# Kernel optimization log

Hardware: AMD Instinct MI355X
Metric: run time of the kernel (lower is better)

## Reference

```python
import jax, jax.numpy as jnp
import numpy as np

B, T, C, H, E, K = 4, 2048, 1024, 2048, 8, 2


def setup_inputs() -> dict:
    key = jax.random.key(0)
    ks = jax.random.split(key, 9)
    s = lambda k, shape, fan: jax.random.normal(k, shape, jnp.float32) / np.sqrt(fan)
    return {
        "x": jax.random.normal(ks[0], (B, T, C), jnp.float32),
        "gate_w": s(ks[1], (C, E), C),            # router gate (no bias)
        "sg_w": s(ks[2], (C, H), C),              # shared expert: gate proj
        "su_w": s(ks[3], (C, H), C),              # shared expert: up proj
        "sd_w": s(ks[4], (H, C), H),              # shared expert: down proj
        "eg_w": s(ks[5], (E, C, H), C),           # routed experts: gate proj
        "eu_w": s(ks[6], (E, C, H), C),           # routed experts: up proj
        "ed_w": s(ks[7], (E, H, C), H),           # routed experts: down proj
    }


def _swiglu(x, wg, wu, wd):
    # x: (B,T,C) -> (B,T,C)
    return jnp.einsum("bth,hc->btc", jax.nn.silu(jnp.einsum("btc,ch->bth", x, wg)) * jnp.einsum("btc,ch->bth", x, wu), wd)


def reference(x, gate_w, sg_w, su_w, sd_w, eg_w, eu_w, ed_w):
    # Router: top-k over expert logits, softmax over selected logits
    logits = jnp.einsum("btc,ce->bte", x, gate_w)            # (B,T,E)
    topk_logits, topk_idx = jax.lax.top_k(logits, K)         # (B,T,K)
    weights = jax.nn.softmax(topk_logits, axis=-1)           # (B,T,K)
    # Dense per-expert combine weight: w_e[b,t,e] = sum_k weights*(idx==e)
    onehot = jax.nn.one_hot(topk_idx, E, dtype=x.dtype)      # (B,T,K,E)
    dense_w = jnp.einsum("btk,btke->bte", weights, onehot)   # (B,T,E)

    shared_out = _swiglu(x, sg_w, su_w, sd_w)

    # Scan over experts (small fixed E), accumulating weighted expert outputs.
    dense_w_e = jnp.moveaxis(dense_w, -1, 0)                 # (E,B,T)

    def step(acc, params):
        wg, wu, wd, w = params
        return acc + w[..., None] * _swiglu(x, wg, wu, wd), None

    expert_out, _ = jax.lax.scan(step, jnp.zeros_like(x), (eg_w, eu_w, ed_w, dense_w_e))
    return shared_out + expert_out, logits
```

## Files before the change

kernel.cpp:

```cpp
#include <hip/hip_runtime.h>
#include <cstdint>
#include <cstddef>

#define NTOK 8192
#define CDIM 1024
#define HDIM 2048
#define NEXP 8
#define NSEG 9
#define MAXTILES 104

typedef __bf16 bf16;
typedef unsigned short u16;
typedef __attribute__((ext_vector_type(8))) __bf16 bf16x8;
typedef __attribute__((ext_vector_type(4))) float f32x4;

__device__ __forceinline__ u16 f2bf(float f) {
  union { u16 u; __bf16 b; } cv;
  cv.b = (__bf16)f;
  return cv.u;
}

__device__ __forceinline__ void gload_lds16(const bf16* g, bf16* l) {
  __builtin_amdgcn_global_load_lds(
      (const __attribute__((address_space(1))) unsigned int*)g,
      (__attribute__((address_space(3))) unsigned int*)l, 16, 0, 0);
}

__global__ __launch_bounds__(64) void init_kernel(int* __restrict__ counts,
                                                  int* __restrict__ fill) {
  if (threadIdx.x < NEXP) {
    counts[threadIdx.x] = 0;
    fill[threadIdx.x] = 0;
  }
}

__global__ __launch_bounds__(256) void cast_x_kernel(
    const float* __restrict__ src, bf16* __restrict__ dst) {
  size_t i = ((size_t)blockIdx.x * 256 + threadIdx.x) * 8;
  float4 a = *(const float4*)(src + i);
  float4 b = *(const float4*)(src + i + 4);
  bf16x8 p;
  p[0] = (bf16)a.x; p[1] = (bf16)a.y; p[2] = (bf16)a.z; p[3] = (bf16)a.w;
  p[4] = (bf16)b.x; p[5] = (bf16)b.y; p[6] = (bf16)b.z; p[7] = (bf16)b.w;
  *(bf16x8*)(dst + i) = p;
}

__global__ __launch_bounds__(256) void router2_kernel(
    const float* __restrict__ x, const float* __restrict__ gw,
    float* __restrict__ logits_out, int* __restrict__ tk_e,
    float* __restrict__ tk_w, int* __restrict__ counts) {
  int wv = threadIdx.x >> 6, l = threadIdx.x & 63;
  int t = blockIdx.x * 4 + wv;
  const float* xr = x + (size_t)t * CDIM;
  float acc[NEXP];
#pragma unroll
  for (int e = 0; e < NEXP; ++e) acc[e] = 0.f;
  for (int c = l; c < CDIM; c += 64) {
    float xv = xr[c];
    const float* g = gw + (size_t)c * NEXP;
    float4 g0 = *(const float4*)(g);
    float4 g1 = *(const float4*)(g + 4);
    acc[0] += xv * g0.x; acc[1] += xv * g0.y; acc[2] += xv * g0.z; acc[3] += xv * g0.w;
    acc[4] += xv * g1.x; acc[5] += xv * g1.y; acc[6] += xv * g1.z; acc[7] += xv * g1.w;
  }
#pragma unroll
  for (int off = 32; off > 0; off >>= 1) {
#pragma unroll
    for (int e = 0; e < NEXP; ++e) acc[e] += __shfl_xor(acc[e], off, 64);
  }
  int e0 = 0; float l0 = acc[0];
#pragma unroll
  for (int e = 1; e < NEXP; ++e) { if (acc[e] > l0) { l0 = acc[e]; e0 = e; } }
  int e1 = -1; float l1 = -3.4e38f;
#pragma unroll
  for (int e = 0; e < NEXP; ++e) { if (e != e0 && acc[e] > l1) { l1 = acc[e]; e1 = e; } }
  float ex = expf(l1 - l0);
  float w0 = 1.f / (1.f + ex), w1 = ex / (1.f + ex);
  if (l < NEXP) logits_out[(size_t)t * NEXP + l] = acc[l];
  if (l == 0) {
    tk_e[2 * t] = e0; tk_e[2 * t + 1] = e1;
    tk_w[2 * t] = w0; tk_w[2 * t + 1] = w1;
    atomicAdd(&counts[e0], 1);
    atomicAdd(&counts[e1], 1);
  }
}

__global__ __launch_bounds__(256) void offsets_kernel(
    const int* __restrict__ counts, int* __restrict__ offs_g,
    int* __restrict__ tile_seg, int* __restrict__ list_tok) {
  __shared__ int off[NSEG], pad[NSEG], cnt[NSEG], ntot;
  int tid = threadIdx.x;
  if (tid == 0) {
    int tot = 0;
    for (int e = 0; e < NSEG; ++e) {
      int c = (e < NEXP) ? counts[e] : NTOK;
      cnt[e] = c; off[e] = tot;
      int p = (c + 255) & ~255;
      pad[e] = p; tot += p;
    }
    ntot = tot;
  }
  __syncthreads();
  if (tid < NSEG) offs_g[tid] = off[tid];
  for (int gt = tid; gt < MAXTILES; gt += 256) {
    int row = gt * 256, seg = -1;
    if (row < ntot) {
      for (int e = 0; e < NSEG; ++e)
        if (row >= off[e] && row < off[e] + pad[e]) { seg = e; break; }
    }
    tile_seg[gt] = seg;
  }
  for (int e = 0; e < NSEG; ++e)
    for (int i = off[e] + cnt[e] + tid; i < off[e] + pad[e]; i += 256)
      list_tok[i] = 0;
}

__global__ __launch_bounds__(256) void scatter_kernel(
    const int* __restrict__ tk_e, const int* __restrict__ offs,
    int* __restrict__ fill, int* __restrict__ list_tok,
    int* __restrict__ inv) {
  int t = blockIdx.x * 256 + threadIdx.x;
  int e0 = tk_e[2 * t], e1 = tk_e[2 * t + 1];
  int p0 = atomicAdd(&fill[e0], 1);
  int i0 = offs[e0] + p0;
  list_tok[i0] = t; inv[2 * t] = i0;
  int p1 = atomicAdd(&fill[e1], 1);
  int i1 = offs[e1] + p1;
  list_tok[i1] = t; inv[2 * t + 1] = i1;
  list_tok[offs[NEXP] + t] = t;
}

__device__ __forceinline__ void transpose_body(const float* __restrict__ src,
                                               u16* __restrict__ dst, int R, int C) {
  __shared__ uint32_t t32[64 * 33];
  const int tid = threadIdx.x;
  const int r0 = blockIdx.y * 64, c0 = blockIdx.x * 64;
  const int rp = tid >> 3;
  const int cg = tid & 7;
  const float* s0 = src + (size_t)(r0 + 2 * rp) * C + c0 + 8 * cg;
  const float* s1 = s0 + C;
  float4 a0 = *(const float4*)(s0);
  float4 a1 = *(const float4*)(s0 + 4);
  float4 b0 = *(const float4*)(s1);
  float4 b1 = *(const float4*)(s1 + 4);
  uint32_t p[8];
  p[0] = f2bf(a0.x) | ((uint32_t)f2bf(b0.x) << 16);
  p[1] = f2bf(a0.y) | ((uint32_t)f2bf(b0.y) << 16);
  p[2] = f2bf(a0.z) | ((uint32_t)f2bf(b0.z) << 16);
  p[3] = f2bf(a0.w) | ((uint32_t)f2bf(b0.w) << 16);
  p[4] = f2bf(a1.x) | ((uint32_t)f2bf(b1.x) << 16);
  p[5] = f2bf(a1.y) | ((uint32_t)f2bf(b1.y) << 16);
  p[6] = f2bf(a1.z) | ((uint32_t)f2bf(b1.z) << 16);
  p[7] = f2bf(a1.w) | ((uint32_t)f2bf(b1.w) << 16);
#pragma unroll
  for (int c = 0; c < 8; ++c) t32[(8 * cg + c) * 33 + rp] = p[c];
  __syncthreads();
  const int oc = tid >> 2, og = tid & 3;
  const uint32_t* rb = &t32[oc * 33 + 8 * og];
  union { uint32_t w[8]; uint4 v[2]; } u;
#pragma unroll
  for (int k = 0; k < 8; ++k) u.w[k] = rb[k];
  u16* d = dst + (size_t)(c0 + oc) * R + r0 + 16 * og;
  *(uint4*)d = u.v[0];
  *(uint4*)(d + 8) = u.v[1];
}

__global__ __launch_bounds__(256) void transpose_cast_kernel(
    const float* __restrict__ src, u16* __restrict__ dst, int R, int C) {
  transpose_body(src, dst, R, C);
}

__global__ __launch_bounds__(256) void transpose_gu_kernel(
    const float* __restrict__ sg, const float* __restrict__ su,
    const float* __restrict__ eg, const float* __restrict__ eu,
    u16* __restrict__ wTg, u16* __restrict__ wTu) {
  const size_t slot = (size_t)HDIM * CDIM;
  int z = blockIdx.z;
  const float* src; u16* dst;
  if (z == 0)       { src = sg;                 dst = wTg + 8 * slot; }
  else if (z == 1)  { src = su;                 dst = wTu + 8 * slot; }
  else if (z < 10)  { src = eg + (z - 2) * slot;  dst = wTg + (z - 2) * slot; }
  else              { src = eu + (z - 10) * slot; dst = wTu + (z - 10) * slot; }
  transpose_body(src, dst, CDIM, HDIM);
}

__global__ __launch_bounds__(256) void transpose_d_kernel(
    const float* __restrict__ sd, const float* __restrict__ ed,
    u16* __restrict__ wTd) {
  const size_t slot = (size_t)HDIM * CDIM;
  int z = blockIdx.z;
  const float* src; u16* dst;
  if (z == 0) { src = sd;                 dst = wTd + 8 * slot; }
  else        { src = ed + (z - 1) * slot; dst = wTd + (z - 1) * slot; }
  transpose_body(src, dst, HDIM, CDIM);
}


__global__ __launch_bounds__(512, 2) void gemm_gu4(
    const bf16* __restrict__ xb, const bf16* __restrict__ wTg,
    const bf16* __restrict__ wTu, const int* __restrict__ tile_seg,
    const int* __restrict__ list_tok, bf16* __restrict__ act) {
  __shared__ __align__(16) bf16 sS[2][32768];
  __shared__ int tokLds[256];

  const int nwg = gridDim.x;
  const int bid = blockIdx.x;
  const int wid = (bid & 7) * (nwg >> 3) + (bid >> 3);
  const int tileIdx = wid % MAXTILES;
  const int colIdx = wid / MAXTILES;
  const int seg = tile_seg[tileIdx];
  if (seg < 0) return;

  const int tid = threadIdx.x, l = tid & 63, wv = tid >> 6;
  const int wr = wv >> 2, wn = wv & 3;
  const int n0 = colIdx * 128;
  const size_t rowbase = (size_t)tileIdx * 256;

  if (tid < 256) tokLds[tid] = list_tok[rowbase + tid];
  __syncthreads();

  const int row8 = tid >> 3;
  const int scol = (((tid & 7) ^ (row8 & 7)) << 3);
  const bf16* gA0 = xb + (size_t)tokLds[row8] * CDIM + scol;
  const bf16* gA1 = xb + (size_t)tokLds[128 + row8] * CDIM + scol;
  const bf16* gA2 = xb + (size_t)tokLds[64 + row8] * CDIM + scol;
  const bf16* gA3 = xb + (size_t)tokLds[192 + row8] * CDIM + scol;
  const size_t wslot = (size_t)seg * HDIM * CDIM;
  const bf16* gBg = wTg + wslot + (size_t)(n0 + row8) * CDIM + scol;
  const bf16* gBu = wTu + wslot + (size_t)(n0 + row8) * CDIM + scol;
  const int t8 = tid * 8;

  const int fr = l & 15, kq = l >> 4;
  const int cS0 = ((kq ^ (l & 7)) << 4);
  const int cS1 = (((4 | kq) ^ (l & 7)) << 4);
  const int aBase = (wr * 128 + fr) * 128;
  const int gBase = 32768 + (wn * 32 + fr) * 128;
  const int uBase = 49152 + (wn * 32 + fr) * 128;

  f32x4 accG[2][4][2], accU[2][4][2];
#pragma unroll
  for (int h = 0; h < 2; ++h)
#pragma unroll
    for (int i = 0; i < 4; ++i)
#pragma unroll
      for (int j = 0; j < 2; ++j) {
        accG[h][i][j] = (f32x4){0.f, 0.f, 0.f, 0.f};
        accU[h][i][j] = (f32x4){0.f, 0.f, 0.f, 0.f};
      }

  auto stC0 = [&](int b, int k0) { bf16* d = &sS[b][0];
    gload_lds16(gBg + k0, d + 16384 + t8);
    gload_lds16(gBg + 64 * CDIM + k0, d + 20480 + t8); };
  auto stC1 = [&](int b, int k0) { bf16* d = &sS[b][0];
    gload_lds16(gA0 + k0, d + t8);
    gload_lds16(gA1 + k0, d + 8192 + t8); };
  auto stC2 = [&](int b, int k0) { bf16* d = &sS[b][0];
    gload_lds16(gBu + k0, d + 24576 + t8);
    gload_lds16(gBu + 64 * CDIM + k0, d + 28672 + t8); };
  auto stC3 = [&](int b, int k0) { bf16* d = &sS[b][0];
    gload_lds16(gA2 + k0, d + 4096 + t8);
    gload_lds16(gA3 + k0, d + 12288 + t8); };

  constexpr int NKT = CDIM / 64;
  stC0(0, 0); stC1(0, 0); stC2(0, 0); stC3(0, 0);

  for (int kt = 0; kt < NKT; ++kt) {
    const int b = kt & 1, bn = b ^ 1;
    const int kn = (kt + 1) * 64;
    const bool more = (kt + 1 < NKT);
    const char* pS = (const char*)&sS[b][0];
    bf16x8 af[4][2], bg[2][2], bu[2][2];

    asm volatile("s_waitcnt vmcnt(4)" ::: "memory");
    __builtin_amdgcn_s_barrier();
#pragma unroll
    for (int i = 0; i < 4; ++i) {
      af[i][0] = *(const bf16x8*)(pS + aBase + i * 2048 + cS0);
      af[i][1] = *(const bf16x8*)(pS + aBase + i * 2048 + cS1);
    }
#pragma unroll
    for (int j = 0; j < 2; ++j) {
      bg[j][0] = *(const bf16x8*)(pS + gBase + j * 2048 + cS0);
      bg[j][1] = *(const bf16x8*)(pS + gBase + j * 2048 + cS1);
    }
    if (more) stC0(bn, kn);
    asm volatile("s_waitcnt lgkmcnt(0)" ::: "memory");
    __builtin_amdgcn_sched_barrier(0);
    __builtin_amdgcn_s_setprio(1);
#pragma unroll
    for (int i = 0; i < 4; ++i)
#pragma unroll
      for (int j = 0; j < 2; ++j) {
        accG[0][i][j] = __builtin_amdgcn_mfma_f32_16x16x32_bf16(af[i][0], bg[j][0], accG[0][i][j], 0, 0, 0);
        accG[0][i][j] = __builtin_amdgcn_mfma_f32_16x16x32_bf16(af[i][1], bg[j][1], accG[0][i][j], 0, 0, 0);
      }
    __builtin_amdgcn_s_setprio(0);

    if (more) asm volatile("s_waitcnt vmcnt(4)" ::: "memory");
    else      asm volatile("s_waitcnt vmcnt(2)" ::: "memory");
    __builtin_amdgcn_s_barrier();
#pragma unroll
    for (int j = 0; j < 2; ++j) {
      bu[j][0] = *(const bf16x8*)(pS + uBase + j * 2048 + cS0);
      bu[j][1] = *(const bf16x8*)(pS + uBase + j * 2048 + cS1);
    }
    if (more) stC1(bn, kn);
    asm volatile("s_waitcnt lgkmcnt(0)" ::: "memory");
    __builtin_amdgcn_sched_barrier(0);
    __builtin_amdgcn_s_setprio(1);
#pragma unroll
    for (int i = 0; i < 4; ++i)
#pragma unroll
      for (int j = 0; j < 2; ++j) {
        accU[0][i][j] = __builtin_amdgcn_mfma_f32_16x16x32_bf16(af[i][0], bu[j][0], accU[0][i][j], 0, 0, 0);
        accU[0][i][j] = __builtin_amdgcn_mfma_f32_16x16x32_bf16(af[i][1], bu[j][1], accU[0][i][j], 0, 0, 0);
      }
    __builtin_amdgcn_s_setprio(0);

    if (more) asm volatile("s_waitcnt vmcnt(4)" ::: "memory");
    else      asm volatile("s_waitcnt vmcnt(0)" ::: "memory");
    __builtin_amdgcn_s_barrier();
#pragma unroll
    for (int i = 0; i < 4; ++i) {
      af[i][0] = *(const bf16x8*)(pS + aBase + 8192 + i * 2048 + cS0);
      af[i][1] = *(const bf16x8*)(pS + aBase + 8192 + i * 2048 + cS1);
    }
    if (more) stC2(bn, kn);
    asm volatile("s_waitcnt lgkmcnt(0)" ::: "memory");
    __builtin_amdgcn_sched_barrier(0);
    __builtin_amdgcn_s_setprio(1);
#pragma unroll
    for (int i = 0; i < 4; ++i)
#pragma unroll
      for (int j = 0; j < 2; ++j) {
        accG[1][i][j] = __builtin_amdgcn_mfma_f32_16x16x32_bf16(af[i][0], bg[j][0], accG[1][i][j], 0, 0, 0);
        accG[1][i][j] = __builtin_amdgcn_mfma_f32_16x16x32_bf16(af[i][1], bg[j][1], accG[1][i][j], 0, 0, 0);
      }
    __builtin_amdgcn_s_setprio(0);

    __builtin_amdgcn_s_barrier();
    if (more) stC3(bn, kn);
    __builtin_amdgcn_s_setprio(1);
#pragma unroll
    for (int i = 0; i < 4; ++i)
#pragma unroll
      for (int j = 0; j < 2; ++j) {
        accU[1][i][j] = __builtin_amdgcn_mfma_f32_16x16x32_bf16(af[i][0], bu[j][0], accU[1][i][j], 0, 0, 0);
        accU[1][i][j] = __builtin_amdgcn_mfma_f32_16x16x32_bf16(af[i][1], bu[j][1], accU[1][i][j], 0, 0, 0);
      }
    __builtin_amdgcn_s_setprio(0);
  }

  const int cn = n0 + wn * 32 + fr;
  const int rb = wr * 128 + kq * 4;
#pragma unroll
  for (int h = 0; h < 2; ++h)
#pragma unroll
    for (int i = 0; i < 4; ++i)
#pragma unroll
      for (int r = 0; r < 4; ++r) {
        const size_t row = rowbase + rb + h * 64 + i * 16 + r;
#pragma unroll
        for (int j = 0; j < 2; ++j) {
          float g = accG[h][i][j][r], uu = accU[h][i][j][r];
          float s = g / (1.f + expf(-g));
          act[row * HDIM + cn + j * 16] = (bf16)(s * uu);
        }
      }
}

__global__ __launch_bounds__(512, 2) void gemm_down4(
    const bf16* __restrict__ act, const bf16* __restrict__ wTd,
    const int* __restrict__ tile_seg, bf16* __restrict__ dbuf) {
  __shared__ __align__(16) bf16 sS[2][24576];

  const int nwg = gridDim.x;
  const int bid = blockIdx.x;
  const int wid = (bid & 7) * (nwg >> 3) + (bid >> 3);
  const int tileIdx = wid % MAXTILES;
  const int colIdx = wid / MAXTILES;
  const int seg = tile_seg[tileIdx];
  if (seg < 0) return;

  const int tid = threadIdx.x, l = tid & 63, wv = tid >> 6;
  const int wr = wv >> 2, wn = wv & 3;
  const int n0 = colIdx * 128;
  const size_t rowbase = (size_t)tileIdx * 256;

  const int row8 = tid >> 3;
  const int scol = (((tid & 7) ^ (row8 & 7)) << 3);
  const bf16* gA0 = act + (rowbase + row8) * HDIM + scol;
  const bf16* gA1 = act + (rowbase + 128 + row8) * HDIM + scol;
  const bf16* gA2 = act + (rowbase + 64 + row8) * HDIM + scol;
  const bf16* gA3 = act + (rowbase + 192 + row8) * HDIM + scol;
  const bf16* gB  = wTd + (size_t)seg * CDIM * HDIM + (size_t)(n0 + row8) * HDIM + scol;
  const int t8 = tid * 8;

  const int fr = l & 15, kq = l >> 4;
  const int cS0 = ((kq ^ (l & 7)) << 4);
  const int cS1 = (((4 | kq) ^ (l & 7)) << 4);
  const int aBase = (wr * 128 + fr) * 128;
  const int bBase = 32768 + (wn * 32 + fr) * 128;

  f32x4 acc[2][4][2];
#pragma unroll
  for (int h = 0; h < 2; ++h)
#pragma unroll
    for (int i = 0; i < 4; ++i)
#pragma unroll
      for (int j = 0; j < 2; ++j) acc[h][i][j] = (f32x4){0.f, 0.f, 0.f, 0.f};

  auto stC0 = [&](int b, int k0) { bf16* d = &sS[b][0];
    gload_lds16(gB + k0, d + 16384 + t8);
    gload_lds16(gB + 64 * HDIM + k0, d + 20480 + t8); };
  auto stC1 = [&](int b, int k0) { bf16* d = &sS[b][0];
    gload_lds16(gA0 + k0, d + t8);
    gload_lds16(gA1 + k0, d + 8192 + t8); };
  auto stC2 = [&](int b, int k0) { bf16* d = &sS[b][0];
    gload_lds16(gA2 + k0, d + 4096 + t8);
    gload_lds16(gA3 + k0, d + 12288 + t8); };

  constexpr int NKT = HDIM / 64;
  stC0(0, 0); stC1(0, 0); stC2(0, 0);

  for (int kt = 0; kt < NKT; ++kt) {
    const int b = kt & 1, bn = b ^ 1;
    const int kn = (kt + 1) * 64;
    const bool more = (kt + 1 < NKT);
    const char* pS = (const char*)&sS[b][0];
    bf16x8 af[4][2], bf[2][2];

    asm volatile("s_waitcnt vmcnt(2)" ::: "memory");
    __builtin_amdgcn_s_barrier();
#pragma unroll
    for (int i = 0; i < 4; ++i) {
      af[i][0] = *(const bf16x8*)(pS + aBase + i * 2048 + cS0);
      af[i][1] = *(const bf16x8*)(pS + aBase + i * 2048 + cS1);
    }
#pragma unroll
    for (int j = 0; j < 2; ++j) {
      bf[j][0] = *(const bf16x8*)(pS + bBase + j * 2048 + cS0);
      bf[j][1] = *(const bf16x8*)(pS + bBase + j * 2048 + cS1);
    }
    if (more) { stC0(bn, kn); stC1(bn, kn); }
    asm volatile("s_waitcnt lgkmcnt(0)" ::: "memory");
    __builtin_amdgcn_sched_barrier(0);
    __builtin_amdgcn_s_setprio(1);
#pragma unroll
    for (int i = 0; i < 4; ++i)
#pragma unroll
      for (int j = 0; j < 2; ++j) {
        acc[0][i][j] = __builtin_amdgcn_mfma_f32_16x16x32_bf16(af[i][0], bf[j][0], acc[0][i][j], 0, 0, 0);
        acc[0][i][j] = __builtin_amdgcn_mfma_f32_16x16x32_bf16(af[i][1], bf[j][1], acc[0][i][j], 0, 0, 0);
      }
    __builtin_amdgcn_s_setprio(0);

    if (more) asm volatile("s_waitcnt vmcnt(4)" ::: "memory");
    else      asm volatile("s_waitcnt vmcnt(0)" ::: "memory");
    __builtin_amdgcn_s_barrier();
#pragma unroll
    for (int i = 0; i < 4; ++i) {
      af[i][0] = *(const bf16x8*)(pS + aBase + 8192 + i * 2048 + cS0);
      af[i][1] = *(const bf16x8*)(pS + aBase + 8192 + i * 2048 + cS1);
    }
    if (more) stC2(bn, kn);
    asm volatile("s_waitcnt lgkmcnt(0)" ::: "memory");
    __builtin_amdgcn_sched_barrier(0);
    __builtin_amdgcn_s_setprio(1);
#pragma unroll
    for (int i = 0; i < 4; ++i)
#pragma unroll
      for (int j = 0; j < 2; ++j) {
        acc[1][i][j] = __builtin_amdgcn_mfma_f32_16x16x32_bf16(af[i][0], bf[j][0], acc[1][i][j], 0, 0, 0);
        acc[1][i][j] = __builtin_amdgcn_mfma_f32_16x16x32_bf16(af[i][1], bf[j][1], acc[1][i][j], 0, 0, 0);
      }
    __builtin_amdgcn_s_setprio(0);
  }

  const int cn = n0 + wn * 32 + fr;
  const int rb = wr * 128 + kq * 4;
#pragma unroll
  for (int h = 0; h < 2; ++h)
#pragma unroll
    for (int i = 0; i < 4; ++i)
#pragma unroll
      for (int r = 0; r < 4; ++r) {
        const size_t row = rowbase + rb + h * 64 + i * 16 + r;
#pragma unroll
        for (int j = 0; j < 2; ++j)
          dbuf[row * CDIM + cn + j * 16] = (bf16)acc[h][i][j][r];
      }
}

__global__ __launch_bounds__(128) void combine_kernel(
    const bf16* __restrict__ dbuf, const int* __restrict__ offs,
    const int* __restrict__ inv, const float* __restrict__ tk_w,
    float* __restrict__ out) {
  const int t = blockIdx.x;
  const int c = threadIdx.x * 8;
  const int rsh = offs[NEXP] + t;
  const int i0 = inv[2 * t], i1 = inv[2 * t + 1];
  const float w0 = tk_w[2 * t], w1 = tk_w[2 * t + 1];
  bf16x8 a = *(const bf16x8*)(dbuf + (size_t)rsh * CDIM + c);
  bf16x8 b = *(const bf16x8*)(dbuf + (size_t)i0 * CDIM + c);
  bf16x8 d = *(const bf16x8*)(dbuf + (size_t)i1 * CDIM + c);
  float* op = out + (size_t)t * CDIM + c;
#pragma unroll
  for (int j = 0; j < 8; ++j)
    op[j] = (float)a[j] + w0 * (float)b[j] + w1 * (float)d[j];
}

__global__ __launch_bounds__(256) void router_kernel(
    const float* __restrict__ x, const float* __restrict__ gw,
    float* __restrict__ dense_w, float* __restrict__ logits_out) {
  int wv = threadIdx.x >> 6, l = threadIdx.x & 63;
  int t = blockIdx.x * 4 + wv;
  const float* xr = x + (size_t)t * CDIM;
  float acc[NEXP];
#pragma unroll
  for (int e = 0; e < NEXP; ++e) acc[e] = 0.f;
  for (int c = l; c < CDIM; c += 64) {
    float xv = xr[c];
    const float* g = gw + (size_t)c * NEXP;
    float4 g0 = *(const float4*)(g);
    float4 g1 = *(const float4*)(g + 4);
    acc[0] += xv * g0.x; acc[1] += xv * g0.y; acc[2] += xv * g0.z; acc[3] += xv * g0.w;
    acc[4] += xv * g1.x; acc[5] += xv * g1.y; acc[6] += xv * g1.z; acc[7] += xv * g1.w;
  }
#pragma unroll
  for (int off = 32; off > 0; off >>= 1) {
#pragma unroll
    for (int e = 0; e < NEXP; ++e) acc[e] += __shfl_xor(acc[e], off, 64);
  }
  int e0 = 0; float l0 = acc[0];
#pragma unroll
  for (int e = 1; e < NEXP; ++e) { if (acc[e] > l0) { l0 = acc[e]; e0 = e; } }
  int e1 = -1; float l1 = -3.4e38f;
#pragma unroll
  for (int e = 0; e < NEXP; ++e) { if (e != e0 && acc[e] > l1) { l1 = acc[e]; e1 = e; } }
  float ex = expf(l1 - l0);
  float w0 = 1.f / (1.f + ex), w1 = ex / (1.f + ex);
  if (l < NEXP) {
    dense_w[(size_t)t * NEXP + l] = (l == e0) ? w0 : ((l == e1) ? w1 : 0.f);
    logits_out[(size_t)t * NEXP + l] = acc[l];
  }
}

template <int MODE>
__global__ __launch_bounds__(256) void gemm_bt(
    const bf16* __restrict__ A, const bf16* __restrict__ Bt,
    int K, int N,
    bf16* __restrict__ Dbf, const bf16* __restrict__ Gin,
    float* __restrict__ outAcc, const float* __restrict__ denseW, int expertId) {
  __shared__ __align__(16) bf16 sA[128 * 32];
  __shared__ __align__(16) bf16 sB[128 * 32];
  const int tid = threadIdx.x;
  const int l = tid & 63, wv = tid >> 6;
  const int wr = wv >> 1, wc = wv & 1;
  const int m0 = blockIdx.y * 128, n0 = blockIdx.x * 128;
  f32x4 acc[4][4];
#pragma unroll
  for (int i = 0; i < 4; ++i)
#pragma unroll
    for (int j = 0; j < 4; ++j) acc[i][j] = (f32x4){0.f, 0.f, 0.f, 0.f};
  const int srow = wv * 16 + (l >> 2);
  const int scol = (l & 3) * 8;
  const bf16* gA = A + (size_t)(m0 + srow) * K + scol;
  const bf16* gB = Bt + (size_t)(n0 + srow) * K + scol;
  bf16* lA = sA + srow * 32 + scol;
  bf16* lB = sB + srow * 32 + scol;
  const int fr = l & 15, fk = (l >> 4) * 8;
  const bf16* rA = sA + (size_t)(wr * 64 + fr) * 32 + fk;
  const bf16* rB = sB + (size_t)(wc * 64 + fr) * 32 + fk;
  for (int k0 = 0; k0 < K; k0 += 32) {
    __syncthreads();
    gload_lds16(gA, lA);
    gload_lds16(gA + (size_t)64 * K, lA + 64 * 32);
    gload_lds16(gB, lB);
    gload_lds16(gB + (size_t)64 * K, lB + 64 * 32);
    gA += 32; gB += 32;
    __syncthreads();
    bf16x8 af[4], bfr[4];
#pragma unroll
    for (int i = 0; i < 4; ++i) af[i] = *(const bf16x8*)(rA + i * 16 * 32);
#pragma unroll
    for (int j = 0; j < 4; ++j) bfr[j] = *(const bf16x8*)(rB + j * 16 * 32);
#pragma unroll
    for (int i = 0; i < 4; ++i)
#pragma unroll
      for (int j = 0; j < 4; ++j)
        acc[i][j] = __builtin_amdgcn_mfma_f32_16x16x32_bf16(af[i], bfr[j], acc[i][j], 0, 0, 0);
  }
  const int cn = n0 + wc * 64 + (l & 15);
  const int rb = m0 + wr * 64 + (l >> 4) * 4;
#pragma unroll
  for (int i = 0; i < 4; ++i)
#pragma unroll
    for (int r = 0; r < 4; ++r) {
      const int m = rb + i * 16 + r;
#pragma unroll
      for (int j = 0; j < 4; ++j) {
        const int n = cn + j * 16;
        float v = acc[i][j][r];
        if (MODE == 0) {
          Dbf[(size_t)m * N + n] = (bf16)v;
        } else if (MODE == 1) {
          float g = (float)Gin[(size_t)m * N + n];
          float s = g / (1.f + expf(-g));
          Dbf[(size_t)m * N + n] = (bf16)(s * v);
        } else if (MODE == 2) {
          outAcc[(size_t)m * N + n] = v;
        } else {
          float w = denseW[(size_t)m * NEXP + expertId];
          outAcc[(size_t)m * N + n] += w * v;
        }
      }
    }
}

extern "C" void kernel_launch(void* const* d_in, const int* in_sizes, int n_in,
                              void* d_out, int out_size, void* d_ws, size_t ws_size,
                              hipStream_t stream) {
  const float* x    = (const float*)d_in[0];
  const float* gate = (const float*)d_in[1];
  const float* sg   = (const float*)d_in[2];
  const float* su   = (const float*)d_in[3];
  const float* sd   = (const float*)d_in[4];
  const float* eg   = (const float*)d_in[5];
  const float* eu   = (const float*)d_in[6];
  const float* ed   = (const float*)d_in[7];
  float* out    = (float*)d_out;
  float* logits = out + (size_t)NTOK * CDIM;

  const size_t MB = 1u << 20;
  const size_t full_need = 226 * MB;

  if (ws_size >= full_need) {
    char* ws = (char*)d_ws;
    bf16*  xb   = (bf16*)(ws);
    bf16*  wTg  = (bf16*)(ws + 16 * MB);
    bf16*  wTu  = (bf16*)(ws + 52 * MB);
    bf16*  act  = (bf16*)(ws + 88 * MB);
    bf16*  wTd  = (bf16*)(ws);
    bf16*  dbuf = (bf16*)(ws + 36 * MB);
    char*  sm   = ws + 200 * MB;
    int*   list_tok = (int*)(sm);
    int*   inv      = (int*)(sm + 128 * 1024);
    int*   tk_e     = (int*)(sm + 256 * 1024);
    float* tk_w     = (float*)(sm + 320 * 1024);
    int*   tile_seg = (int*)(sm + 384 * 1024);
    int*   counts   = (int*)(sm + 388 * 1024);
    int*   fill     = (int*)(sm + 389 * 1024);
    int*   offs     = (int*)(sm + 390 * 1024);

    init_kernel<<<1, 64, 0, stream>>>(counts, fill);
    cast_x_kernel<<<NTOK * CDIM / (256 * 8), 256, 0, stream>>>(x, xb);
    router2_kernel<<<NTOK / 4, 256, 0, stream>>>(x, gate, logits, tk_e, tk_w, counts);
    offsets_kernel<<<1, 256, 0, stream>>>(counts, offs, tile_seg, list_tok);
    scatter_kernel<<<NTOK / 256, 256, 0, stream>>>(tk_e, offs, fill, list_tok, inv);

    dim3 tgu(HDIM / 64, CDIM / 64, 18);
    transpose_gu_kernel<<<tgu, 256, 0, stream>>>(sg, su, eg, eu, (u16*)wTg, (u16*)wTu);

    gemm_gu4<<<(HDIM / 128) * MAXTILES, 512, 0, stream>>>(xb, wTg, wTu, tile_seg, list_tok, act);

    dim3 tdd(CDIM / 64, HDIM / 64, 9);
    transpose_d_kernel<<<tdd, 256, 0, stream>>>(sd, ed, (u16*)wTd);

    gemm_down4<<<(CDIM / 128) * MAXTILES, 512, 0, stream>>>(act, wTd, tile_seg, dbuf);
    combine_kernel<<<NTOK, 128, 0, stream>>>(dbuf, offs, inv, tk_w, out);
    return;
  }

  char* ws = (char*)d_ws;
  bf16*  xb   = (bf16*)(ws);
  bf16*  wTgf = (bf16*)(ws + 16 * MB);
  bf16*  wTuf = (bf16*)(ws + 20 * MB);
  bf16*  wTdf = (bf16*)(ws + 24 * MB);
  bf16*  gbuf = (bf16*)(ws + 28 * MB);
  float* dw   = (float*)(ws + 60 * MB);
  if (ws_size < 60 * MB + (size_t)NTOK * NEXP * sizeof(float)) return;

  cast_x_kernel<<<NTOK * CDIM / (256 * 8), 256, 0, stream>>>(x, xb);
  router_kernel<<<NTOK / 4, 256, 0, stream>>>(x, gate, dw, logits);

  dim3 tg1(HDIM / 64, CDIM / 64);
  dim3 tg2(CDIM / 64, HDIM / 64);
  dim3 g1(HDIM / 128, NTOK / 128);
  dim3 g2(CDIM / 128, NTOK / 128);

  transpose_cast_kernel<<<tg1, 256, 0, stream>>>(sg, (u16*)wTgf, CDIM, HDIM);
  transpose_cast_kernel<<<tg1, 256, 0, stream>>>(su, (u16*)wTuf, CDIM, HDIM);
  transpose_cast_kernel<<<tg2, 256, 0, stream>>>(sd, (u16*)wTdf, HDIM, CDIM);
  gemm_bt<0><<<g1, 256, 0, stream>>>(xb, wTgf, CDIM, HDIM, gbuf, nullptr, nullptr, nullptr, 0);
  gemm_bt<1><<<g1, 256, 0, stream>>>(xb, wTuf, CDIM, HDIM, gbuf, gbuf, nullptr, nullptr, 0);
  gemm_bt<2><<<g2, 256, 0, stream>>>(gbuf, wTdf, HDIM, CDIM, nullptr, nullptr, out, nullptr, 0);

  for (int e = 0; e < NEXP; ++e) {
    const float* egp = eg + (size_t)e * CDIM * HDIM;
    const float* eup = eu + (size_t)e * CDIM * HDIM;
    const float* edp = ed + (size_t)e * HDIM * CDIM;
    transpose_cast_kernel<<<tg1, 256, 0, stream>>>(egp, (u16*)wTgf, CDIM, HDIM);
    transpose_cast_kernel<<<tg1, 256, 0, stream>>>(eup, (u16*)wTuf, CDIM, HDIM);
    transpose_cast_kernel<<<tg2, 256, 0, stream>>>(edp, (u16*)wTdf, HDIM, CDIM);
    gemm_bt<0><<<g1, 256, 0, stream>>>(xb, wTgf, CDIM, HDIM, gbuf, nullptr, nullptr, nullptr, 0);
    gemm_bt<1><<<g1, 256, 0, stream>>>(xb, wTuf, CDIM, HDIM, gbuf, gbuf, nullptr, nullptr, 0);
    gemm_bt<3><<<g2, 256, 0, stream>>>(gbuf, wTdf, HDIM, CDIM, nullptr, nullptr, out, dw, e);
  }
}
```

Baseline: 917.8 us.

## Stage full k-tile upfront per iteration and widen down-proj GEMM tile to 256 columns

Both grouped GEMMs now issue all global-to-LDS loads for the next k-tile at the top of each iteration, then wait and barrier once. Previously the loads were split into four staggered chunks interleaved with the MFMA phases. The down-projection kernel also doubles its N tile from 128 to 256 columns, which halves the grid and the number of times the activation rows are re-read. That adds accumulator registers and LDS per block. The coarser staging reduces barriers but may expose more load latency, and the larger tile risks register pressure at the same occupancy target.

```diff
diff --git a/kernel.cpp b/kernel.cpp
--- a/kernel.cpp
+++ b/kernel.cpp
@@ -196,7 +196,13 @@
 }
 
 
-__global__ __launch_bounds__(512, 2) void gemm_gu4(
+#define PHASE_READS_BEGIN __builtin_amdgcn_sched_barrier(0)
+#define PHASE_COMPUTE     asm volatile("s_waitcnt lgkmcnt(0)" ::: "memory"); \
+                          __builtin_amdgcn_sched_barrier(0);                 \
+                          __builtin_amdgcn_s_setprio(1)
+#define PHASE_END         __builtin_amdgcn_s_setprio(0)
+
+__global__ __launch_bounds__(512, 2) void gemm_gu5(
     const bf16* __restrict__ xb, const bf16* __restrict__ wTg,
     const bf16* __restrict__ wTu, const int* __restrict__ tile_seg,
     const int* __restrict__ list_tok, bf16* __restrict__ act) {
@@ -222,8 +228,8 @@
   const int row8 = tid >> 3;
   const int scol = (((tid & 7) ^ (row8 & 7)) << 3);
   const bf16* gA0 = xb + (size_t)tokLds[row8] * CDIM + scol;
-  const bf16* gA1 = xb + (size_t)tokLds[128 + row8] * CDIM + scol;
-  const bf16* gA2 = xb + (size_t)tokLds[64 + row8] * CDIM + scol;
+  const bf16* gA1 = xb + (size_t)tokLds[64 + row8] * CDIM + scol;
+  const bf16* gA2 = xb + (size_t)tokLds[128 + row8] * CDIM + scol;
   const bf16* gA3 = xb + (size_t)tokLds[192 + row8] * CDIM + scol;
   const size_t wslot = (size_t)seg * HDIM * CDIM;
   const bf16* gBg = wTg + wslot + (size_t)(n0 + row8) * CDIM + scol;
@@ -248,31 +254,33 @@
         accU[h][i][j] = (f32x4){0.f, 0.f, 0.f, 0.f};
       }
 
-  auto stC0 = [&](int b, int k0) { bf16* d = &sS[b][0];
+  auto stage_all = [&](int b, int k0) {
+    bf16* d = &sS[b][0];
+    gload_lds16(gA0 + k0, d + t8);
+    gload_lds16(gA1 + k0, d + 4096 + t8);
+    gload_lds16(gA2 + k0, d + 8192 + t8);
+    gload_lds16(gA3 + k0, d + 12288 + t8);
     gload_lds16(gBg + k0, d + 16384 + t8);
-    gload_lds16(gBg + 64 * CDIM + k0, d + 20480 + t8); };
-  auto stC1 = [&](int b, int k0) { bf16* d = &sS[b][0];
-    gload_lds16(gA0 + k0, d + t8);
-    gload_lds16(gA1 + k0, d + 8192 + t8); };
-  auto stC2 = [&](int b, int k0) { bf16* d = &sS[b][0];
+    gload_lds16(gBg + 64 * CDIM + k0, d + 20480 + t8);
     gload_lds16(gBu + k0, d + 24576 + t8);
-    gload_lds16(gBu + 64 * CDIM + k0, d + 28672 + t8); };
-  auto stC3 = [&](int b, int k0) { bf16* d = &sS[b][0];
-    gload_lds16(gA2 + k0, d + 4096 + t8);
-    gload_lds16(gA3 + k0, d + 12288 + t8); };
+    gload_lds16(gBu + 64 * CDIM + k0, d + 28672 + t8);
+  };
 
   constexpr int NKT = CDIM / 64;
-  stC0(0, 0); stC1(0, 0); stC2(0, 0); stC3(0, 0);
+  stage_all(0, 0);
 
   for (int kt = 0; kt < NKT; ++kt) {
     const int b = kt & 1, bn = b ^ 1;
-    const int kn = (kt + 1) * 64;
     const bool more = (kt + 1 < NKT);
+    __builtin_amdgcn_s_barrier();
+    if (more) stage_all(bn, (kt + 1) * 64);
+    if (more) asm volatile("s_waitcnt vmcnt(8)" ::: "memory");
+    else      asm volatile("s_waitcnt vmcnt(0)" ::: "memory");
+    __builtin_amdgcn_s_barrier();
     const char* pS = (const char*)&sS[b][0];
     bf16x8 af[4][2], bg[2][2], bu[2][2];
 
-    asm volatile("s_waitcnt vmcnt(4)" ::: "memory");
-    __builtin_amdgcn_s_barrier();
+    PHASE_READS_BEGIN;
 #pragma unroll
     for (int i = 0; i < 4; ++i) {
       af[i][0] = *(const bf16x8*)(pS + aBase + i * 2048 + cS0);
@@ -283,10 +291,7 @@
       bg[j][0] = *(const bf16x8*)(pS + gBase + j * 2048 + cS0);
       bg[j][1] = *(const bf16x8*)(pS + gBase + j * 2048 + cS1);
     }
-    if (more) stC0(bn, kn);
-    asm volatile("s_waitcnt lgkmcnt(0)" ::: "memory");
-    __builtin_amdgcn_sched_barrier(0);
-    __builtin_amdgcn_s_setprio(1);
+    PHASE_COMPUTE;
 #pragma unroll
     for (int i = 0; i < 4; ++i)
 #pragma unroll
@@ -294,20 +299,15 @@
         accG[0][i][j] = __builtin_amdgcn_mfma_f32_16x16x32_bf16(af[i][0], bg[j][0], accG[0][i][j], 0, 0, 0);
         accG[0][i][j] = __builtin_amdgcn_mfma_f32_16x16x32_bf16(af[i][1], bg[j][1], accG[0][i][j], 0, 0, 0);
       }
-    __builtin_amdgcn_s_setprio(0);
-
-    if (more) asm volatile("s_waitcnt vmcnt(4)" ::: "memory");
-    else      asm volatile("s_waitcnt vmcnt(2)" ::: "memory");
-    __builtin_amdgcn_s_barrier();
+    PHASE_END;
+
+    PHASE_READS_BEGIN;
 #pragma unroll
     for (int j = 0; j < 2; ++j) {
       bu[j][0] = *(const bf16x8*)(pS + uBase + j * 2048 + cS0);
       bu[j][1] = *(const bf16x8*)(pS + uBase + j * 2048 + cS1);
     }
-    if (more) stC1(bn, kn);
-    asm volatile("s_waitcnt lgkmcnt(0)" ::: "memory");
-    __builtin_amdgcn_sched_barrier(0);
-    __builtin_amdgcn_s_setprio(1);
+    PHASE_COMPUTE;
 #pragma unroll
     for (int i = 0; i < 4; ++i)
 #pragma unroll
@@ -315,20 +315,15 @@
         accU[0][i][j] = __builtin_amdgcn_mfma_f32_16x16x32_bf16(af[i][0], bu[j][0], accU[0][i][j], 0, 0, 0);
         accU[0][i][j] = __builtin_amdgcn_mfma_f32_16x16x32_bf16(af[i][1], bu[j][1], accU[0][i][j], 0, 0, 0);
       }
-    __builtin_amdgcn_s_setprio(0);
-
-    if (more) asm volatile("s_waitcnt vmcnt(4)" ::: "memory");
-    else      asm volatile("s_waitcnt vmcnt(0)" ::: "memory");
-    __builtin_amdgcn_s_barrier();
+    PHASE_END;
+
+    PHASE_READS_BEGIN;
 #pragma unroll
     for (int i = 0; i < 4; ++i) {
       af[i][0] = *(const bf16x8*)(pS + aBase + 8192 + i * 2048 + cS0);
       af[i][1] = *(const bf16x8*)(pS + aBase + 8192 + i * 2048 + cS1);
     }
-    if (more) stC2(bn, kn);
-    asm volatile("s_waitcnt lgkmcnt(0)" ::: "memory");
-    __builtin_amdgcn_sched_barrier(0);
-    __builtin_amdgcn_s_setprio(1);
+    PHASE_COMPUTE;
 #pragma unroll
     for (int i = 0; i < 4; ++i)
 #pragma unroll
@@ -336,10 +331,8 @@
         accG[1][i][j] = __builtin_amdgcn_mfma_f32_16x16x32_bf16(af[i][0], bg[j][0], accG[1][i][j], 0, 0, 0);
         accG[1][i][j] = __builtin_amdgcn_mfma_f32_16x16x32_bf16(af[i][1], bg[j][1], accG[1][i][j], 0, 0, 0);
       }
-    __builtin_amdgcn_s_setprio(0);
-
-    __builtin_amdgcn_s_barrier();
-    if (more) stC3(bn, kn);
+    PHASE_END;
+
     __builtin_amdgcn_s_setprio(1);
 #pragma unroll
     for (int i = 0; i < 4; ++i)
@@ -369,10 +362,10 @@
       }
 }
 
-__global__ __launch_bounds__(512, 2) void gemm_down4(
+__global__ __launch_bounds__(512, 2) void gemm_down5(
     const bf16* __restrict__ act, const bf16* __restrict__ wTd,
     const int* __restrict__ tile_seg, bf16* __restrict__ dbuf) {
-  __shared__ __align__(16) bf16 sS[2][24576];
+  __shared__ __align__(16) bf16 sS[2][32768];
 
   const int nwg = gridDim.x;
   const int bid = blockIdx.x;
@@ -384,14 +377,14 @@
 
   const int tid = threadIdx.x, l = tid & 63, wv = tid >> 6;
   const int wr = wv >> 2, wn = wv & 3;
-  const int n0 = colIdx * 128;
+  const int n0 = colIdx * 256;
   const size_t rowbase = (size_t)tileIdx * 256;
 
   const int row8 = tid >> 3;
   const int scol = (((tid & 7) ^ (row8 & 7)) << 3);
   const bf16* gA0 = act + (rowbase + row8) * HDIM + scol;
-  const bf16* gA1 = act + (rowbase + 128 + row8) * HDIM + scol;
-  const bf16* gA2 = act + (rowbase + 64 + row8) * HDIM + scol;
+  const bf16* gA1 = act + (rowbase + 64 + row8) * HDIM + scol;
+  const bf16* gA2 = act + (rowbase + 128 + row8) * HDIM + scol;
   const bf16* gA3 = act + (rowbase + 192 + row8) * HDIM + scol;
   const bf16* gB  = wTd + (size_t)seg * CDIM * HDIM + (size_t)(n0 + row8) * HDIM + scol;
   const int t8 = tid * 8;
@@ -400,38 +393,45 @@
   const int cS0 = ((kq ^ (l & 7)) << 4);
   const int cS1 = (((4 | kq) ^ (l & 7)) << 4);
   const int aBase = (wr * 128 + fr) * 128;
-  const int bBase = 32768 + (wn * 32 + fr) * 128;
-
-  f32x4 acc[2][4][2];
+  const int bBase = 32768 + (wn * 64 + fr) * 128;
+
+  f32x4 acc[2][2][4][2];
 #pragma unroll
   for (int h = 0; h < 2; ++h)
 #pragma unroll
-    for (int i = 0; i < 4; ++i)
-#pragma unroll
-      for (int j = 0; j < 2; ++j) acc[h][i][j] = (f32x4){0.f, 0.f, 0.f, 0.f};
-
-  auto stC0 = [&](int b, int k0) { bf16* d = &sS[b][0];
+    for (int nh = 0; nh < 2; ++nh)
+#pragma unroll
+      for (int i = 0; i < 4; ++i)
+#pragma unroll
+        for (int j = 0; j < 2; ++j) acc[h][nh][i][j] = (f32x4){0.f, 0.f, 0.f, 0.f};
+
+  auto stage_all = [&](int b, int k0) {
+    bf16* d = &sS[b][0];
+    gload_lds16(gA0 + k0, d + t8);
+    gload_lds16(gA1 + k0, d + 4096 + t8);
+    gload_lds16(gA2 + k0, d + 8192 + t8);
+    gload_lds16(gA3 + k0, d + 12288 + t8);
     gload_lds16(gB + k0, d + 16384 + t8);
-    gload_lds16(gB + 64 * HDIM + k0, d + 20480 + t8); };
-  auto stC1 = [&](int b, int k0) { bf16* d = &sS[b][0];
-    gload_lds16(gA0 + k0, d + t8);
-    gload_lds16(gA1 + k0, d + 8192 + t8); };
-  auto stC2 = [&](int b, int k0) { bf16* d = &sS[b][0];
-    gload_lds16(gA2 + k0, d + 4096 + t8);
-    gload_lds16(gA3 + k0, d + 12288 + t8); };
+    gload_lds16(gB + 64 * HDIM + k0, d + 20480 + t8);
+    gload_lds16(gB + 128 * HDIM + k0, d + 24576 + t8);
+    gload_lds16(gB + 192 * HDIM + k0, d + 28672 + t8);
+  };
 
   constexpr int NKT = HDIM / 64;
-  stC0(0, 0); stC1(0, 0); stC2(0, 0);
+  stage_all(0, 0);
 
   for (int kt = 0; kt < NKT; ++kt) {
     const int b = kt & 1, bn = b ^ 1;
-    const int kn = (kt + 1) * 64;
     const bool more = (kt + 1 < NKT);
+    __builtin_amdgcn_s_barrier();
+    if (more) stage_all(bn, (kt + 1) * 64);
+    if (more) asm volatile("s_waitcnt vmcnt(8)" ::: "memory");
+    else      asm volatile("s_waitcnt vmcnt(0)" ::: "memory");
+    __builtin_amdgcn_s_barrier();
     const char* pS = (const char*)&sS[b][0];
-    bf16x8 af[4][2], bf[2][2];
-
-    asm volatile("s_waitcnt vmcnt(2)" ::: "memory");
-    __builtin_amdgcn_s_barrier();
+    bf16x8 af[4][2], bfr[2][2][2];
+
+    PHASE_READS_BEGIN;
 #pragma unroll
     for (int i = 0; i < 4; ++i) {
       af[i][0] = *(const bf16x8*)(pS + aBase + i * 2048 + cS0);
@@ -439,45 +439,62 @@
     }
 #pragma unroll
     for (int j = 0; j < 2; ++j) {
-      bf[j][0] = *(const bf16x8*)(pS + bBase + j * 2048 + cS0);
-      bf[j][1] = *(const bf16x8*)(pS + bBase + j * 2048 + cS1);
-    }
-    if (more) { stC0(bn, kn); stC1(bn, kn); }
-    asm volatile("s_waitcnt lgkmcnt(0)" ::: "memory");
-    __builtin_amdgcn_sched_barrier(0);
-    __builtin_amdgcn_s_setprio(1);
-#pragma unroll
-    for (int i = 0; i < 4; ++i)
-#pragma unroll
-      for (int j = 0; j < 2; ++j) {
-        acc[0][i][j] = __builtin_amdgcn_mfma_f32_16x16x32_bf16(af[i][0], bf[j][0], acc[0][i][j], 0, 0, 0);
-        acc[0][i][j] = __builtin_amdgcn_mfma_f32_16x16x32_bf16(af[i][1], bf[j][1], acc[0][i][j], 0, 0, 0);
-      }
-    __builtin_amdgcn_s_setprio(0);
-
-    if (more) asm volatile("s_waitcnt vmcnt(4)" ::: "memory");
-    else      asm volatile("s_waitcnt vmcnt(0)" ::: "memory");
-    __builtin_amdgcn_s_barrier();
+      bfr[0][j][0] = *(const bf16x8*)(pS + bBase + j * 2048 + cS0);
+      bfr[0][j][1] = *(const bf16x8*)(pS + bBase + j * 2048 + cS1);
+    }
+    PHASE_COMPUTE;
+#pragma unroll
+    for (int i = 0; i < 4; ++i)
+#pragma unroll
+      for (int j = 0; j < 2; ++j) {
+        acc[0][0][i][j] = __builtin_amdgcn_mfma_f32_16x16x32_bf16(af[i][0], bfr[0][j][0], acc[0][0][i][j], 0, 0, 0);
+        acc[0][0][i][j] = __builtin_amdgcn_mfma_f32_16x16x32_bf16(af[i][1], bfr[0][j][1], acc[0][0][i][j], 0, 0, 0);
+      }
+    PHASE_END;
+
+    PHASE_READS_BEGIN;
+#pragma unroll
+    for (int j = 0; j < 2; ++j) {
+      bfr[1][j][0] = *(const bf16x8*)(pS + bBase + 4096 + j * 2048 + cS0);
+      bfr[1][j][1] = *(const bf16x8*)(pS + bBase + 4096 + j * 2048 + cS1);
+    }
+    PHASE_COMPUTE;
+#pragma unroll
+    for (int i = 0; i < 4; ++i)
+#pragma unroll
+      for (int j = 0; j < 2; ++j) {
+        acc[0][1][i][j] = __builtin_amdgcn_mfma_f32_16x16x32_bf16(af[i][0], bfr[1][j][0], acc[0][1][i][j], 0, 0, 0);
+        acc[0][1][i][j] = __builtin_amdgcn_mfma_f32_16x16x32_bf16(af[i][1], bfr[1][j][1], acc[0][1][i][j], 0, 0, 0);
+      }
+    PHASE_END;
+
+    PHASE_READS_BEGIN;
 #pragma unroll
     for (int i = 0; i < 4; ++i) {
       af[i][0] = *(const bf16x8*)(pS + aBase + 8192 + i * 2048 + cS0);
       af[i][1] = *(const bf16x8*)(pS + aBase + 8192 + i * 2048 + cS1);
     }
-    if (more) stC2(bn, kn);
-    asm volatile("s_waitcnt lgkmcnt(0)" ::: "memory");
-    __builtin_amdgcn_sched_barrier(0);
+    PHASE_COMPUTE;
+#pragma unroll
+    for (int i = 0; i < 4; ++i)
+#pragma unroll
+      for (int j = 0; j < 2; ++j) {
+        acc[1][0][i][j] = __builtin_amdgcn_mfma_f32_16x16x32_bf16(af[i][0], bfr[0][j][0], acc[1][0][i][j], 0, 0, 0);
+        acc[1][0][i][j] = __builtin_amdgcn_mfma_f32_16x16x32_bf16(af[i][1], bfr[0][j][1], acc[1][0][i][j], 0, 0, 0);
+      }
+    PHASE_END;
+
     __builtin_amdgcn_s_setprio(1);
 #pragma unroll
     for (int i = 0; i < 4; ++i)
 #pragma unroll
       for (int j = 0; j < 2; ++j) {
-        acc[1][i][j] = __builtin_amdgcn_mfma_f32_16x16x32_bf16(af[i][0], bf[j][0], acc[1][i][j], 0, 0, 0);
-        acc[1][i][j] = __builtin_amdgcn_mfma_f32_16x16x32_bf16(af[i][1], bf[j][1], acc[1][i][j], 0, 0, 0);
+        acc[1][1][i][j] = __builtin_amdgcn_mfma_f32_16x16x32_bf16(af[i][0], bfr[1][j][0], acc[1][1][i][j], 0, 0, 0);
+        acc[1][1][i][j] = __builtin_amdgcn_mfma_f32_16x16x32_bf16(af[i][1], bfr[1][j][1], acc[1][1][i][j], 0, 0, 0);
       }
     __builtin_amdgcn_s_setprio(0);
   }
 
-  const int cn = n0 + wn * 32 + fr;
   const int rb = wr * 128 + kq * 4;
 #pragma unroll
   for (int h = 0; h < 2; ++h)
@@ -487,8 +504,10 @@
       for (int r = 0; r < 4; ++r) {
         const size_t row = rowbase + rb + h * 64 + i * 16 + r;
 #pragma unroll
-        for (int j = 0; j < 2; ++j)
-          dbuf[row * CDIM + cn + j * 16] = (bf16)acc[h][i][j][r];
+        for (int nh = 0; nh < 2; ++nh)
+#pragma unroll
+          for (int j = 0; j < 2; ++j)
+            dbuf[row * CDIM + n0 + wn * 64 + nh * 32 + j * 16 + fr] = (bf16)acc[h][nh][i][j][r];
       }
 }
 
@@ -662,12 +681,12 @@
     dim3 tgu(HDIM / 64, CDIM / 64, 18);
     transpose_gu_kernel<<<tgu, 256, 0, stream>>>(sg, su, eg, eu, (u16*)wTg, (u16*)wTu);
 
-    gemm_gu4<<<(HDIM / 128) * MAXTILES, 512, 0, stream>>>(xb, wTg, wTu, tile_seg, list_tok, act);
+    gemm_gu5<<<(HDIM / 128) * MAXTILES, 512, 0, stream>>>(xb, wTg, wTu, tile_seg, list_tok, act);
 
     dim3 tdd(CDIM / 64, HDIM / 64, 9);
     transpose_d_kernel<<<tdd, 256, 0, stream>>>(sd, ed, (u16*)wTd);
 
-    gemm_down4<<<(CDIM / 128) * MAXTILES, 512, 0, stream>>>(act, wTd, tile_seg, dbuf);
+    gemm_down5<<<(CDIM / 256) * MAXTILES, 512, 0, stream>>>(act, wTd, tile_seg, dbuf);
     combine_kernel<<<NTOK, 128, 0, stream>>>(dbuf, offs, inv, tk_w, out);
     return;
   }
```

Measured after the change: 941.7 us. 2.6% more time.
